# Optimization experiments

Measured on AMD Instinct MI355X. Metric: run time of the kernel, lower is better.

## Reference

```python
import jax, jax.numpy as jnp
import numpy as np

D = 1024
H = 16
DH = D // H
DFF = 4096
EPS = 1e-5


def new_gelu(u):
    # HF NewGELUActivation: 0.5*u*(1+tanh(sqrt(2/pi)*(u+0.044715*u^3)))
    c = np.sqrt(2.0 / np.pi).astype(np.float32)
    return 0.5 * u * (1.0 + jnp.tanh(c * (u + 0.044715 * u ** 3)))


def layer_norm(u, g, b):
    mu = jnp.mean(u, axis=-1, keepdims=True)
    var = jnp.mean((u - mu) ** 2, axis=-1, keepdims=True)
    return (u - mu) * jax.lax.rsqrt(var + EPS) * g + b


def setup_inputs() -> dict:
    key = jax.random.key(0)
    ks = jax.random.split(key, 12)
    s = 0.02
    inp = {
        "x": jax.random.normal(ks[0], (4, 1024, D), dtype=jnp.float32),
        "Wq": jax.random.normal(ks[1], (D, D), dtype=jnp.float32) * s,
        "bq": jnp.zeros((D,), jnp.float32),
        "Wk": jax.random.normal(ks[2], (D, D), dtype=jnp.float32) * s,
        "bk": jnp.zeros((D,), jnp.float32),
        "Wv": jax.random.normal(ks[3], (D, D), dtype=jnp.float32) * s,
        "bv": jnp.zeros((D,), jnp.float32),
        "Wo": jax.random.normal(ks[4], (D, D), dtype=jnp.float32) * s,
        "bo": jnp.zeros((D,), jnp.float32),
        "g1": jnp.ones((D,), jnp.float32),
        "b1": jnp.zeros((D,), jnp.float32),
        "W1": jax.random.normal(ks[5], (D, DFF), dtype=jnp.float32) * s,
        "bm1": jnp.zeros((DFF,), jnp.float32),
        "W2": jax.random.normal(ks[6], (DFF, D), dtype=jnp.float32) * s,
        "bm2": jnp.zeros((D,), jnp.float32),
        "g2": jnp.ones((D,), jnp.float32),
        "b2": jnp.zeros((D,), jnp.float32),
    }
    return inp


def reference(x, Wq, bq, Wk, bk, Wv, bv, Wo, bo, g1, b1, W1, bm1, W2, bm2, g2, b2):
    B, S, _ = x.shape
    q = (x @ Wq + bq).reshape(B, S, H, DH)
    k = (x @ Wk + bk).reshape(B, S, H, DH)
    v = (x @ Wv + bv).reshape(B, S, H, DH)
    scores = jnp.einsum("bshd,bthd->bhst", q, k) / np.sqrt(DH).astype(np.float32)
    probs = jax.nn.softmax(scores, axis=-1)
    attn = jnp.einsum("bhst,bthd->bshd", probs, v).reshape(B, S, D)
    attn = attn @ Wo + bo
    x1 = layer_norm(x + attn, g1, b1)
    mlp = new_gelu(x1 @ W1 + bm1) @ W2 + bm2
    out = layer_norm(x1 + mlp, g2, b2)
    return out
```

## Files before the change

kernel.cpp:

```cpp
#include <hip/hip_runtime.h>

#define D_    1024
#define HH    16
#define DHEAD 64
#define DFF_  4096
#define NTOK  4096
#define SQLEN 1024

typedef unsigned short ushort_t;
typedef __attribute__((ext_vector_type(8))) short short8;
typedef __attribute__((ext_vector_type(4))) float floatx4;

#define LOG2E 1.44269504f

__device__ __forceinline__ unsigned short f2bf(float f) {
  union { float f; unsigned u; } x; x.f = f;
  unsigned r = x.u + 0x7fffu + ((x.u >> 16) & 1u);
  return (unsigned short)(r >> 16);
}
__device__ __forceinline__ float bf2f(unsigned short u) {
  union { unsigned u; float f; } x; x.u = ((unsigned)u) << 16;
  return x.f;
}
__device__ __forceinline__ unsigned pack2bf(float a, float b) {
  return (unsigned)f2bf(a) | ((unsigned)f2bf(b) << 16);
}
__device__ __forceinline__ float fast_exp2(float x) {
  return __builtin_amdgcn_exp2f(x);
}
__device__ __forceinline__ float fast_gelu(float u) {
  float u2 = u * u;
  float arg = u * (2.30220414f + 0.10294307f * u2);
  float e = __builtin_amdgcn_exp2f(arg);
  float r = __builtin_amdgcn_rcpf(e + 1.0f);
  return u - u * r;
}

__device__ __forceinline__ void async_ld16(const void* g, void* l) {
  __builtin_amdgcn_global_load_lds(
      (const __attribute__((address_space(1))) unsigned int*)g,
      (__attribute__((address_space(3))) unsigned int*)l, 16, 0, 0);
}

__global__ __launch_bounds__(256) void cast_x_kernel(const float* __restrict__ x,
                                                     ushort_t* __restrict__ xb) {
  int i = blockIdx.x * 256 + threadIdx.x;
  float4 v = ((const float4*)x)[i];
  ushort4 o;
  o.x = f2bf(v.x); o.y = f2bf(v.y); o.z = f2bf(v.z); o.w = f2bf(v.w);
  ((ushort4*)xb)[i] = o;
}

__global__ __launch_bounds__(256) void transpose_cast4_kernel(
    const float* __restrict__ Wa, const float* __restrict__ Wb,
    const float* __restrict__ Wc, const float* __restrict__ Wd,
    ushort_t* __restrict__ Ta, ushort_t* __restrict__ Tb,
    ushort_t* __restrict__ Tc, ushort_t* __restrict__ Td) {
  __shared__ float tile[32][33];
  int z = blockIdx.z;
  const float* W = (z == 0) ? Wa : (z == 1) ? Wb : (z == 2) ? Wc : Wd;
  ushort_t* T = (z == 0) ? Ta : (z == 1) ? Tb : (z == 2) ? Tc : Td;
  int n0 = blockIdx.x * 32, k0 = blockIdx.y * 32;
  int tx = threadIdx.x & 31, ty = threadIdx.x >> 5;
#pragma unroll
  for (int i = 0; i < 4; i++)
    tile[ty + i * 8][tx] = W[(size_t)(k0 + ty + i * 8) * D_ + n0 + tx];
  __syncthreads();
#pragma unroll
  for (int i = 0; i < 4; i++)
    T[(size_t)(n0 + ty + i * 8) * D_ + k0 + tx] = f2bf(tile[tx][ty + i * 8]);
}

__global__ __launch_bounds__(256) void transpose_cast_kernel(const float* __restrict__ W,
                                                             ushort_t* __restrict__ Wt,
                                                             int K, int N) {
  __shared__ float tile[32][33];
  int n0 = blockIdx.x * 32, k0 = blockIdx.y * 32;
  int tx = threadIdx.x & 31, ty = threadIdx.x >> 5;
#pragma unroll
  for (int i = 0; i < 4; i++)
    tile[ty + i * 8][tx] = W[(size_t)(k0 + ty + i * 8) * N + n0 + tx];
  __syncthreads();
#pragma unroll
  for (int i = 0; i < 4; i++)
    Wt[(size_t)(n0 + ty + i * 8) * K + k0 + tx] = f2bf(tile[tx][ty + i * 8]);
}

template <int MODE>
__global__ __launch_bounds__(256) void gemm_bf16(
    const ushort_t* __restrict__ A, const ushort_t* __restrict__ Bt,
    int M, int N, int K, int Ks, int nb,
    const float* __restrict__ bias0, const float* __restrict__ bias1,
    const float* __restrict__ bias2,
    ushort_t* __restrict__ o0, ushort_t* __restrict__ o1, ushort_t* __restrict__ o2) {
  __shared__ alignas(16) ushort_t sA[128 * 32];
  __shared__ alignas(16) ushort_t sB[128 * 32];
  int tid = threadIdx.x;
  int w = tid >> 6, lane = tid & 63, quad = lane >> 4, l16 = lane & 15;
  int wm = w >> 1, wn = w & 1;

  int sp = blockIdx.x / nb;
  int bid = blockIdx.x - sp * nb;
  int gridN = N >> 7;
  int T = nb >> 3;
  int lin = (bid & 7) * T + (bid >> 3);
  int ng = gridN << 3;
  int gidx = lin / ng;
  int rem = lin - gidx * ng;
  int m0 = ((gidx << 3) + (rem & 7)) << 7;
  int n0 = (rem >> 3) << 7;
  int kbeg = sp * Ks, kend = kbeg + Ks;

  floatx4 acc[4][4];
#pragma unroll
  for (int i = 0; i < 4; i++)
#pragma unroll
    for (int j = 0; j < 4; j++) acc[i][j] = (floatx4){0.f, 0.f, 0.f, 0.f};

  int rA = tid >> 2;
  int cA = (tid & 3) * 8;
  const ushort_t* gA0 = A + (size_t)(m0 + rA) * K + cA;
  const ushort_t* gA1 = A + (size_t)(m0 + 64 + rA) * K + cA;
  const ushort_t* gB0 = Bt + (size_t)(n0 + rA) * K + cA;
  const ushort_t* gB1 = Bt + (size_t)(n0 + 64 + rA) * K + cA;
  ushort_t* lA0 = sA + (w * 64) * 8;
  ushort_t* lA1 = sA + (256 + w * 64) * 8;
  ushort_t* lB0 = sB + (w * 64) * 8;
  ushort_t* lB1 = sB + (256 + w * 64) * 8;

  for (int k0 = kbeg; k0 < kend; k0 += 32) {
    __syncthreads();
    async_ld16(gA0 + k0, lA0);
    async_ld16(gA1 + k0, lA1);
    async_ld16(gB0 + k0, lB0);
    async_ld16(gB1 + k0, lB1);
    __syncthreads();
    short8 af[4], bfr[4];
#pragma unroll
    for (int mt = 0; mt < 4; mt++)
      af[mt] = *(const short8*)(sA + (wm * 64 + mt * 16 + l16) * 32 + quad * 8);
#pragma unroll
    for (int nt = 0; nt < 4; nt++)
      bfr[nt] = *(const short8*)(sB + (wn * 64 + nt * 16 + l16) * 32 + quad * 8);
#pragma unroll
    for (int mt = 0; mt < 4; mt++)
#pragma unroll
      for (int nt = 0; nt < 4; nt++)
        acc[mt][nt] = __builtin_amdgcn_mfma_f32_16x16x32_bf16(af[mt], bfr[nt],
                                                              acc[mt][nt], 0, 0, 0);
  }

#pragma unroll
  for (int nt = 0; nt < 4; nt++) {
    int cg = n0 + wn * 64 + nt * 16 + l16;
    if (MODE == 0) {
      int sel = cg >> 10, nn = cg & 1023;
      const float* bp = (sel == 0) ? bias0 : ((sel == 1) ? bias1 : bias2);
      float bb = bp[nn];
      int hh = nn >> 6, dd = nn & 63;
#pragma unroll
      for (int mt = 0; mt < 4; mt++) {
        int rg0 = m0 + wm * 64 + mt * 16 + quad * 4;
        int b0 = rg0 >> 10, s0 = rg0 & 1023;
        if (sel == 2) {
          ushort4 ov;
          ov.x = f2bf(acc[mt][nt][0] + bb);
          ov.y = f2bf(acc[mt][nt][1] + bb);
          ov.z = f2bf(acc[mt][nt][2] + bb);
          ov.w = f2bf(acc[mt][nt][3] + bb);
          *(ushort4*)(o2 + ((size_t)(b0 * HH + hh) * DHEAD + dd) * SQLEN + s0) = ov;
        } else {
          ushort_t* dst = sel ? o1 : o0;
          float sc = (sel == 0) ? 0.125f : 1.0f;
#pragma unroll
          for (int r = 0; r < 4; r++)
            dst[((size_t)(b0 * HH + hh) * SQLEN + s0 + r) * DHEAD + dd] =
                f2bf((acc[mt][nt][r] + bb) * sc);
        }
      }
    } else {
      float bb = (MODE == 2) ? bias0[cg & (N - 1)] : 0.f;
#pragma unroll
      for (int mt = 0; mt < 4; mt++) {
#pragma unroll
        for (int r = 0; r < 4; r++) {
          int rg = m0 + wm * 64 + mt * 16 + quad * 4 + r;
          float c = acc[mt][nt][r];
          if (MODE == 2) {
            o0[(size_t)rg * N + cg] = f2bf(fast_gelu(c + bb));
          } else {
            o0[(size_t)sp * M * N + (size_t)rg * N + cg] = f2bf(c);
          }
        }
      }
    }
  }
}

__global__ __launch_bounds__(256) void flash_attn_kernel(const ushort_t* __restrict__ q,
                                                         const ushort_t* __restrict__ k,
                                                         const ushort_t* __restrict__ vt,
                                                         ushort_t* __restrict__ ctx) {
  __shared__ alignas(16) ushort_t sQ[2][64 * 32];
  __shared__ alignas(16) ushort_t sK[2][64 * 32];
  __shared__ alignas(16) ushort_t sVt[2][64 * 32];
  __shared__ alignas(16) ushort_t sP[4][2][16 * 32];
  int tid = threadIdx.x;
  int w = tid >> 6, lane = tid & 63, quad = lane >> 4, l16 = lane & 15;
  int bh = blockIdx.x, qt = blockIdx.y;
  int b_ = bh >> 4, h_ = bh & 15;

  const ushort_t* Qp = q + ((size_t)bh * SQLEN + qt * 64) * DHEAD;
  const ushort_t* Kp = k + (size_t)bh * SQLEN * DHEAD;
  const ushort_t* Vtp = vt + (size_t)bh * DHEAD * SQLEN;

  int srow = lane >> 2, scol8 = (lane & 3) * 8;

#pragma unroll
  for (int t = 0; t < 2; t++) {
    int id = w * 2 + t, panel = id & 1, rg = id >> 1;
    async_ld16(Qp + (rg * 16 + srow) * 64 + panel * 32 + scol8,
               (char*)sQ + panel * 4096 + rg * 1024);
  }

  float m_run = -1e30f, l_run = 0.f;
  floatx4 o_acc[4];
#pragma unroll
  for (int dt = 0; dt < 4; dt++) o_acc[dt] = (floatx4){0.f, 0.f, 0.f, 0.f};

  for (int kt = 0; kt < 16; kt++) {
    __syncthreads();
#pragma unroll
    for (int t = 0; t < 2; t++) {
      int id = w * 2 + t, panel = id & 1, rg = id >> 1;
      int row = rg * 16 + srow, col = panel * 32 + scol8;
      async_ld16(Kp + kt * 64 * 64 + row * 64 + col,
                 (char*)sK + panel * 4096 + rg * 1024);
      async_ld16(Vtp + (size_t)row * SQLEN + kt * 64 + col,
                 (char*)sVt + panel * 4096 + rg * 1024);
    }
    __syncthreads();

    floatx4 st[4];
#pragma unroll
    for (int nt = 0; nt < 4; nt++) st[nt] = (floatx4){0.f, 0.f, 0.f, 0.f};
#pragma unroll
    for (int kc = 0; kc < 2; kc++) {
      short8 aq = *(const short8*)(sQ[kc] + (w * 16 + l16) * 32 + quad * 8);
#pragma unroll
      for (int nt = 0; nt < 4; nt++) {
        short8 kf = *(const short8*)(sK[kc] + (nt * 16 + l16) * 32 + quad * 8);
        st[nt] = __builtin_amdgcn_mfma_f32_16x16x32_bf16(kf, aq, st[nt], 0, 0, 0);
      }
    }

    float tm = -1e30f;
#pragma unroll
    for (int nt = 0; nt < 4; nt++)
#pragma unroll
      for (int r = 0; r < 4; r++) tm = fmaxf(tm, st[nt][r]);
    tm = fmaxf(tm, __shfl_xor(tm, 16));
    tm = fmaxf(tm, __shfl_xor(tm, 32));
    float mnew = fmaxf(m_run, tm);
    float alpha = fast_exp2((m_run - mnew) * LOG2E);
    float rs = 0.f;
    unsigned pk[4][2];
#pragma unroll
    for (int nt = 0; nt < 4; nt++) {
      float p0 = fast_exp2((st[nt][0] - mnew) * LOG2E);
      float p1 = fast_exp2((st[nt][1] - mnew) * LOG2E);
      float p2 = fast_exp2((st[nt][2] - mnew) * LOG2E);
      float p3 = fast_exp2((st[nt][3] - mnew) * LOG2E);
      rs += (p0 + p1) + (p2 + p3);
      pk[nt][0] = pack2bf(p0, p1);
      pk[nt][1] = pack2bf(p2, p3);
    }
    rs += __shfl_xor(rs, 16);
    rs += __shfl_xor(rs, 32);
    l_run = l_run * alpha + rs;
    m_run = mnew;
#pragma unroll
    for (int dt = 0; dt < 4; dt++)
#pragma unroll
      for (int r = 0; r < 4; r++) o_acc[dt][r] *= alpha;

#pragma unroll
    for (int nt = 0; nt < 4; nt++) {
      uint2 d2; d2.x = pk[nt][0]; d2.y = pk[nt][1];
      *(uint2*)((char*)&sP[w][nt >> 1][0] + l16 * 64 + (nt & 1) * 32 + quad * 8) = d2;
    }

#pragma unroll
    for (int kc = 0; kc < 2; kc++) {
      short8 pf = *(const short8*)((char*)&sP[w][kc][0] + l16 * 64 + quad * 16);
#pragma unroll
      for (int dt = 0; dt < 4; dt++) {
        short8 vf = *(const short8*)(sVt[kc] + (dt * 16 + l16) * 32 + quad * 8);
        o_acc[dt] = __builtin_amdgcn_mfma_f32_16x16x32_bf16(vf, pf, o_acc[dt], 0, 0, 0);
      }
    }
  }

  float inv = 1.f / l_run;
  int s_ = qt * 64 + w * 16 + l16;
  ushort_t* cp = ctx + (size_t)(b_ * SQLEN + s_) * D_ + h_ * DHEAD + quad * 4;
#pragma unroll
  for (int dt = 0; dt < 4; dt++) {
    ushort4 ov;
    ov.x = f2bf(o_acc[dt][0] * inv);
    ov.y = f2bf(o_acc[dt][1] * inv);
    ov.z = f2bf(o_acc[dt][2] * inv);
    ov.w = f2bf(o_acc[dt][3] * inv);
    *(ushort4*)(cp + dt * 16) = ov;
  }
}

template <int S, int WB>
__global__ __launch_bounds__(256) void ln_red_kernel(
    const ushort_t* __restrict__ parts, const float* __restrict__ bias,
    const float* __restrict__ res, const float* __restrict__ g,
    const float* __restrict__ b, float* __restrict__ outf,
    ushort_t* __restrict__ outb) {
  int row = blockIdx.x, tid = threadIdx.x;
  float4 v = ((const float4*)(res + (size_t)row * D_))[tid];
  float4 bb = ((const float4*)bias)[tid];
  v.x += bb.x; v.y += bb.y; v.z += bb.z; v.w += bb.w;
#pragma unroll
  for (int s = 0; s < S; s++) {
    ushort4 p = ((const ushort4*)(parts + (size_t)s * NTOK * D_ + (size_t)row * D_))[tid];
    v.x += bf2f(p.x); v.y += bf2f(p.y); v.z += bf2f(p.z); v.w += bf2f(p.w);
  }
  float s1 = v.x + v.y + v.z + v.w;
  float s2 = v.x * v.x + v.y * v.y + v.z * v.z + v.w * v.w;
#pragma unroll
  for (int off = 32; off > 0; off >>= 1) {
    s1 += __shfl_down(s1, off);
    s2 += __shfl_down(s2, off);
  }
  __shared__ float red[10];
  int wid = tid >> 6, lane = tid & 63;
  if (lane == 0) { red[wid] = s1; red[4 + wid] = s2; }
  __syncthreads();
  if (tid == 0) {
    float ts = red[0] + red[1] + red[2] + red[3];
    float ts2 = red[4] + red[5] + red[6] + red[7];
    float mu = ts * (1.f / 1024.f);
    float var = ts2 * (1.f / 1024.f) - mu * mu;
    red[8] = mu;
    red[9] = rsqrtf(var + 1e-5f);
  }
  __syncthreads();
  float mu = red[8], rsg = red[9];
  float4 gv = ((const float4*)g)[tid];
  float4 bv = ((const float4*)b)[tid];
  float4 o;
  o.x = (v.x - mu) * rsg * gv.x + bv.x;
  o.y = (v.y - mu) * rsg * gv.y + bv.y;
  o.z = (v.z - mu) * rsg * gv.z + bv.z;
  o.w = (v.w - mu) * rsg * gv.w + bv.w;
  if (outf) ((float4*)(outf + (size_t)row * D_))[tid] = o;
  if (WB) {
    ushort4 ob;
    ob.x = f2bf(o.x); ob.y = f2bf(o.y); ob.z = f2bf(o.z); ob.w = f2bf(o.w);
    ((ushort4*)(outb + (size_t)row * D_))[tid] = ob;
  }
}

extern "C" void kernel_launch(void* const* d_in, const int* in_sizes, int n_in,
                              void* d_out, int out_size, void* d_ws, size_t ws_size,
                              hipStream_t stream) {
  const float* x   = (const float*)d_in[0];
  const float* Wq  = (const float*)d_in[1];
  const float* bq  = (const float*)d_in[2];
  const float* Wk  = (const float*)d_in[3];
  const float* bk  = (const float*)d_in[4];
  const float* Wv  = (const float*)d_in[5];
  const float* bv  = (const float*)d_in[6];
  const float* Wo  = (const float*)d_in[7];
  const float* bo  = (const float*)d_in[8];
  const float* g1  = (const float*)d_in[9];
  const float* b1  = (const float*)d_in[10];
  const float* W1  = (const float*)d_in[11];
  const float* bm1 = (const float*)d_in[12];
  const float* W2  = (const float*)d_in[13];
  const float* bm2 = (const float*)d_in[14];
  const float* g2  = (const float*)d_in[15];
  const float* b2  = (const float*)d_in[16];
  float* out = (float*)d_out;

  char* ws = (char*)d_ws;
  const size_t MB = 1024 * 1024;
  ushort_t* xb    = (ushort_t*)(ws + 0);
  ushort_t* wqkvt = (ushort_t*)(ws + 8 * MB);
  ushort_t* wot   = (ushort_t*)(ws + 14 * MB);
  ushort_t* w1t   = (ushort_t*)(ws + 16 * MB);
  ushort_t* w2t   = (ushort_t*)(ws + 24 * MB);
  ushort_t* qb    = (ushort_t*)(ws + 32 * MB);
  ushort_t* kb    = (ushort_t*)(ws + 40 * MB);
  ushort_t* vtb   = (ushort_t*)(ws + 48 * MB);
  ushort_t* ctx   = (ushort_t*)(ws + 56 * MB);
  float*    x1    = (float*)   (ws + 64 * MB);
  ushort_t* x1b   = (ushort_t*)(ws + 80 * MB);
  ushort_t* hbuf  = (ushort_t*)(ws + 88 * MB);
  ushort_t* pWo   = (ushort_t*)(ws + 32 * MB);
  ushort_t* pMd   = (ushort_t*)(ws + 32 * MB);
  (void)ws_size; (void)in_sizes; (void)n_in; (void)out_size;

  hipLaunchKernelGGL(cast_x_kernel, dim3(NTOK * D_ / 1024), dim3(256), 0, stream, x, xb);
  hipLaunchKernelGGL(transpose_cast4_kernel, dim3(32, 32, 4), dim3(256), 0, stream,
                     Wq, Wk, Wv, Wo,
                     wqkvt, wqkvt + (size_t)D_ * D_, wqkvt + (size_t)2 * D_ * D_, wot);
  hipLaunchKernelGGL(transpose_cast_kernel, dim3(DFF_ / 32, 32), dim3(256), 0, stream,
                     W1, w1t, D_, DFF_);
  hipLaunchKernelGGL(transpose_cast_kernel, dim3(32, DFF_ / 32), dim3(256), 0, stream,
                     W2, w2t, DFF_, D_);

  hipLaunchKernelGGL((gemm_bf16<0>), dim3(768), dim3(256), 0, stream,
                     xb, wqkvt, NTOK, 3072, D_, D_, 768, bq, bk, bv, qb, kb, vtb);

  hipLaunchKernelGGL(flash_attn_kernel, dim3(4 * HH, SQLEN / 64), dim3(256), 0, stream,
                     qb, kb, vtb, ctx);

  hipLaunchKernelGGL((gemm_bf16<3>), dim3(512), dim3(256), 0, stream,
                     ctx, wot, NTOK, D_, D_, 512, 256,
                     (const float*)nullptr, (const float*)nullptr,
                     (const float*)nullptr, pWo, (ushort_t*)nullptr, (ushort_t*)nullptr);

  hipLaunchKernelGGL((ln_red_kernel<2, 1>), dim3(NTOK), dim3(256), 0, stream,
                     pWo, bo, x, g1, b1, x1, x1b);

  hipLaunchKernelGGL((gemm_bf16<2>), dim3(1024), dim3(256), 0, stream,
                     x1b, w1t, NTOK, DFF_, D_, D_, 1024, bm1, (const float*)nullptr,
                     (const float*)nullptr, hbuf, (ushort_t*)nullptr, (ushort_t*)nullptr);

  hipLaunchKernelGGL((gemm_bf16<3>), dim3(1024), dim3(256), 0, stream,
                     hbuf, w2t, NTOK, D_, DFF_, 1024, 256,
                     (const float*)nullptr, (const float*)nullptr,
                     (const float*)nullptr, pMd, (ushort_t*)nullptr, (ushort_t*)nullptr);

  hipLaunchKernelGGL((ln_red_kernel<4, 0>), dim3(NTOK), dim3(256), 0, stream,
                     pMd, bm2, x1, g2, b2, out, (ushort_t*)nullptr);
}
```

Baseline: 379.7 us.

## Merge prep cast/transpose kernels and double the GEMM K-step per barrier

Folds the x cast and the four weight transpose-cast launches into one prep kernel, which saves launch overhead and lets the pieces run concurrently. The bf16 GEMM now loads two 32-wide K slices per iteration into a two-slab LDS buffer and runs both slices between one pair of barriers. This halves the number of synchronizations per tile but doubles LDS use, which may reduce occupancy. The bias load in MODE 2 also drops a redundant mask.

```diff
diff --git a/kernel.cpp b/kernel.cpp
--- a/kernel.cpp
+++ b/kernel.cpp
@@ -42,48 +42,48 @@
       (__attribute__((address_space(3))) unsigned int*)l, 16, 0, 0);
 }
 
-__global__ __launch_bounds__(256) void cast_x_kernel(const float* __restrict__ x,
-                                                     ushort_t* __restrict__ xb) {
-  int i = blockIdx.x * 256 + threadIdx.x;
-  float4 v = ((const float4*)x)[i];
-  ushort4 o;
-  o.x = f2bf(v.x); o.y = f2bf(v.y); o.z = f2bf(v.z); o.w = f2bf(v.w);
-  ((ushort4*)xb)[i] = o;
-}
-
-__global__ __launch_bounds__(256) void transpose_cast4_kernel(
-    const float* __restrict__ Wa, const float* __restrict__ Wb,
-    const float* __restrict__ Wc, const float* __restrict__ Wd,
-    ushort_t* __restrict__ Ta, ushort_t* __restrict__ Tb,
-    ushort_t* __restrict__ Tc, ushort_t* __restrict__ Td) {
+__global__ __launch_bounds__(256) void prep_kernel(
+    const float* __restrict__ x, const float* __restrict__ Wq,
+    const float* __restrict__ Wk, const float* __restrict__ Wv,
+    const float* __restrict__ Wo, const float* __restrict__ W1,
+    const float* __restrict__ W2,
+    ushort_t* __restrict__ xb, ushort_t* __restrict__ wqkvt,
+    ushort_t* __restrict__ wot, ushort_t* __restrict__ w1t,
+    ushort_t* __restrict__ w2t) {
+  int bid = blockIdx.x, tid = threadIdx.x;
+  if (bid < 4096) {
+    int i = bid * 256 + tid;
+    float4 v = ((const float4*)x)[i];
+    ushort4 o;
+    o.x = f2bf(v.x); o.y = f2bf(v.y); o.z = f2bf(v.z); o.w = f2bf(v.w);
+    ((ushort4*)xb)[i] = o;
+    return;
+  }
   __shared__ float tile[32][33];
-  int z = blockIdx.z;
-  const float* W = (z == 0) ? Wa : (z == 1) ? Wb : (z == 2) ? Wc : Wd;
-  ushort_t* T = (z == 0) ? Ta : (z == 1) ? Tb : (z == 2) ? Tc : Td;
-  int n0 = blockIdx.x * 32, k0 = blockIdx.y * 32;
-  int tx = threadIdx.x & 31, ty = threadIdx.x >> 5;
-#pragma unroll
-  for (int i = 0; i < 4; i++)
-    tile[ty + i * 8][tx] = W[(size_t)(k0 + ty + i * 8) * D_ + n0 + tx];
-  __syncthreads();
-#pragma unroll
-  for (int i = 0; i < 4; i++)
-    T[(size_t)(n0 + ty + i * 8) * D_ + k0 + tx] = f2bf(tile[tx][ty + i * 8]);
-}
-
-__global__ __launch_bounds__(256) void transpose_cast_kernel(const float* __restrict__ W,
-                                                             ushort_t* __restrict__ Wt,
-                                                             int K, int N) {
-  __shared__ float tile[32][33];
-  int n0 = blockIdx.x * 32, k0 = blockIdx.y * 32;
-  int tx = threadIdx.x & 31, ty = threadIdx.x >> 5;
+  const float* W; ushort_t* T; int K, N, n0, k0;
+  if (bid < 8192) {
+    int id = bid - 4096, z = id >> 10, xy = id & 1023;
+    W = (z == 0) ? Wq : (z == 1) ? Wk : (z == 2) ? Wv : Wo;
+    T = (z < 3) ? wqkvt + (size_t)z * D_ * D_ : wot;
+    K = D_; N = D_;
+    n0 = (xy & 31) * 32; k0 = (xy >> 5) * 32;
+  } else if (bid < 12288) {
+    int id = bid - 8192;
+    W = W1; T = w1t; K = D_; N = DFF_;
+    n0 = (id & 127) * 32; k0 = (id >> 7) * 32;
+  } else {
+    int id = bid - 12288;
+    W = W2; T = w2t; K = DFF_; N = D_;
+    n0 = (id & 31) * 32; k0 = (id >> 5) * 32;
+  }
+  int tx = tid & 31, ty = tid >> 5;
 #pragma unroll
   for (int i = 0; i < 4; i++)
     tile[ty + i * 8][tx] = W[(size_t)(k0 + ty + i * 8) * N + n0 + tx];
   __syncthreads();
 #pragma unroll
   for (int i = 0; i < 4; i++)
-    Wt[(size_t)(n0 + ty + i * 8) * K + k0 + tx] = f2bf(tile[tx][ty + i * 8]);
+    T[(size_t)(n0 + ty + i * 8) * K + k0 + tx] = f2bf(tile[tx][ty + i * 8]);
 }
 
 template <int MODE>
@@ -93,8 +93,8 @@
     const float* __restrict__ bias0, const float* __restrict__ bias1,
     const float* __restrict__ bias2,
     ushort_t* __restrict__ o0, ushort_t* __restrict__ o1, ushort_t* __restrict__ o2) {
-  __shared__ alignas(16) ushort_t sA[128 * 32];
-  __shared__ alignas(16) ushort_t sB[128 * 32];
+  __shared__ alignas(16) ushort_t sA[2][128 * 32];
+  __shared__ alignas(16) ushort_t sB[2][128 * 32];
   int tid = threadIdx.x;
   int w = tid >> 6, lane = tid & 63, quad = lane >> 4, l16 = lane & 15;
   int wm = w >> 1, wn = w & 1;
@@ -102,8 +102,8 @@
   int sp = blockIdx.x / nb;
   int bid = blockIdx.x - sp * nb;
   int gridN = N >> 7;
-  int T = nb >> 3;
-  int lin = (bid & 7) * T + (bid >> 3);
+  int Tn = nb >> 3;
+  int lin = (bid & 7) * Tn + (bid >> 3);
   int ng = gridN << 3;
   int gidx = lin / ng;
   int rem = lin - gidx * ng;
@@ -117,37 +117,38 @@
 #pragma unroll
     for (int j = 0; j < 4; j++) acc[i][j] = (floatx4){0.f, 0.f, 0.f, 0.f};
 
-  int rA = tid >> 2;
-  int cA = (tid & 3) * 8;
-  const ushort_t* gA0 = A + (size_t)(m0 + rA) * K + cA;
-  const ushort_t* gA1 = A + (size_t)(m0 + 64 + rA) * K + cA;
-  const ushort_t* gB0 = Bt + (size_t)(n0 + rA) * K + cA;
-  const ushort_t* gB1 = Bt + (size_t)(n0 + 64 + rA) * K + cA;
-  ushort_t* lA0 = sA + (w * 64) * 8;
-  ushort_t* lA1 = sA + (256 + w * 64) * 8;
-  ushort_t* lB0 = sB + (w * 64) * 8;
-  ushort_t* lB1 = sB + (256 + w * 64) * 8;
-
-  for (int k0 = kbeg; k0 < kend; k0 += 32) {
+  int srow = lane >> 2, scol = (lane & 3) * 8;
+  const ushort_t* gA = A + (size_t)(m0 + w * 16 + srow) * K + scol;
+  const ushort_t* gB = Bt + (size_t)(n0 + w * 16 + srow) * K + scol;
+  ushort_t* lA = sA[0] + w * 16 * 32;
+  ushort_t* lB = sB[0] + w * 16 * 32;
+
+  for (int k0 = kbeg; k0 < kend; k0 += 64) {
     __syncthreads();
-    async_ld16(gA0 + k0, lA0);
-    async_ld16(gA1 + k0, lA1);
-    async_ld16(gB0 + k0, lB0);
-    async_ld16(gB1 + k0, lB1);
+#pragma unroll
+    for (int h = 0; h < 2; h++)
+#pragma unroll
+      for (int p = 0; p < 2; p++) {
+        async_ld16(gA + (size_t)h * 64 * K + k0 + p * 32, lA + p * 4096 + h * 2048);
+        async_ld16(gB + (size_t)h * 64 * K + k0 + p * 32, lB + p * 4096 + h * 2048);
+      }
     __syncthreads();
-    short8 af[4], bfr[4];
-#pragma unroll
-    for (int mt = 0; mt < 4; mt++)
-      af[mt] = *(const short8*)(sA + (wm * 64 + mt * 16 + l16) * 32 + quad * 8);
-#pragma unroll
-    for (int nt = 0; nt < 4; nt++)
-      bfr[nt] = *(const short8*)(sB + (wn * 64 + nt * 16 + l16) * 32 + quad * 8);
-#pragma unroll
-    for (int mt = 0; mt < 4; mt++)
+#pragma unroll
+    for (int kc = 0; kc < 2; kc++) {
+      short8 af[4], bfr[4];
+#pragma unroll
+      for (int mt = 0; mt < 4; mt++)
+        af[mt] = *(const short8*)(sA[kc] + (wm * 64 + mt * 16 + l16) * 32 + quad * 8);
 #pragma unroll
       for (int nt = 0; nt < 4; nt++)
-        acc[mt][nt] = __builtin_amdgcn_mfma_f32_16x16x32_bf16(af[mt], bfr[nt],
-                                                              acc[mt][nt], 0, 0, 0);
+        bfr[nt] = *(const short8*)(sB[kc] + (wn * 64 + nt * 16 + l16) * 32 + quad * 8);
+#pragma unroll
+      for (int mt = 0; mt < 4; mt++)
+#pragma unroll
+        for (int nt = 0; nt < 4; nt++)
+          acc[mt][nt] = __builtin_amdgcn_mfma_f32_16x16x32_bf16(af[mt], bfr[nt],
+                                                                acc[mt][nt], 0, 0, 0);
+    }
   }
 
 #pragma unroll
@@ -179,7 +180,7 @@
         }
       }
     } else {
-      float bb = (MODE == 2) ? bias0[cg & (N - 1)] : 0.f;
+      float bb = (MODE == 2) ? bias0[cg] : 0.f;
 #pragma unroll
       for (int mt = 0; mt < 4; mt++) {
 #pragma unroll
@@ -406,14 +407,8 @@
   ushort_t* pMd   = (ushort_t*)(ws + 32 * MB);
   (void)ws_size; (void)in_sizes; (void)n_in; (void)out_size;
 
-  hipLaunchKernelGGL(cast_x_kernel, dim3(NTOK * D_ / 1024), dim3(256), 0, stream, x, xb);
-  hipLaunchKernelGGL(transpose_cast4_kernel, dim3(32, 32, 4), dim3(256), 0, stream,
-                     Wq, Wk, Wv, Wo,
-                     wqkvt, wqkvt + (size_t)D_ * D_, wqkvt + (size_t)2 * D_ * D_, wot);
-  hipLaunchKernelGGL(transpose_cast_kernel, dim3(DFF_ / 32, 32), dim3(256), 0, stream,
-                     W1, w1t, D_, DFF_);
-  hipLaunchKernelGGL(transpose_cast_kernel, dim3(32, DFF_ / 32), dim3(256), 0, stream,
-                     W2, w2t, DFF_, D_);
+  hipLaunchKernelGGL(prep_kernel, dim3(16384), dim3(256), 0, stream,
+                     x, Wq, Wk, Wv, Wo, W1, W2, xb, wqkvt, wot, w1t, w2t);
 
   hipLaunchKernelGGL((gemm_bf16<0>), dim3(768), dim3(256), 0, stream,
                      xb, wqkvt, NTOK, 3072, D_, D_, 768, bq, bk, bv, qb, kb, vtb);
```

New measurement: 350.2 us. 7.8% less time.
